# Performance work log

Measured on AMD Instinct MI355X. Metric: run time of the kernel, lower is better.

Reference implementation:

```python
import jax, jax.numpy as jnp
import numpy as np

D_MODEL = 768
N_HEADS = 12
D_HEAD = 64
INIT_RANGE = 0.02
IGNORE = -100000.0


def setup_inputs() -> dict:
    key = jax.random.key(0)
    ks = jax.random.split(key, 5)
    x = jax.random.normal(ks[0], (2, 2048, D_MODEL), dtype=jnp.float32)
    W_Q = INIT_RANGE * jax.random.normal(ks[1], (N_HEADS, D_MODEL, D_HEAD), dtype=jnp.float32)
    W_K = INIT_RANGE * jax.random.normal(ks[2], (N_HEADS, D_MODEL, D_HEAD), dtype=jnp.float32)
    W_V = INIT_RANGE * jax.random.normal(ks[3], (N_HEADS, D_MODEL, D_HEAD), dtype=jnp.float32)
    W_O = INIT_RANGE * jax.random.normal(ks[4], (N_HEADS, D_HEAD, D_MODEL), dtype=jnp.float32)
    b_Q = jnp.zeros((N_HEADS, D_HEAD), dtype=jnp.float32)
    b_K = jnp.zeros((N_HEADS, D_HEAD), dtype=jnp.float32)
    b_V = jnp.zeros((N_HEADS, D_HEAD), dtype=jnp.float32)
    b_O = jnp.zeros((D_MODEL,), dtype=jnp.float32)
    return {"x": x, "W_Q": W_Q, "b_Q": b_Q, "W_K": W_K, "b_K": b_K,
            "W_V": W_V, "b_V": b_V, "W_O": W_O, "b_O": b_O}


def reference(x, W_Q, b_Q, W_K, b_K, W_V, b_V, W_O, b_O):
    # x: [b, s, m]; W_*: [h, m, d]
    Q = jnp.einsum('bsm,hmd->bshd', x, W_Q) + b_Q  # [b, s, h, d]
    K = jnp.einsum('bsm,hmd->bshd', x, W_K) + b_K
    V = jnp.einsum('bsm,hmd->bshd', x, W_V) + b_V
    scores = jnp.einsum('bqhd,bkhd->bhqk', Q, K) / jnp.sqrt(jnp.float32(D_HEAD))
    s = scores.shape[-1]
    causal = jnp.triu(jnp.ones((s, s), dtype=bool), k=1)  # True above diagonal
    scores = jnp.where(causal, jnp.float32(IGNORE), scores)
    pattern = jax.nn.softmax(scores, axis=-1)  # [b, h, q, k]
    Z = jnp.einsum('bhqk,bkhd->bqhd', pattern, V)
    out = jnp.einsum('bqhd,hdm->bqm', Z, W_O) + b_O
    return out
```

## Files before the change

### kernel.cpp

```cpp
#include <hip/hip_runtime.h>
#include <hip/hip_bf16.h>

#define BATCH 2
#define SLEN 2048
#define NH 12
#define DM 768
#define DH 64
#define ROWS (BATCH*SLEN)
#define NQKV (3*DM)
#define NCHUNK 80

typedef __attribute__((ext_vector_type(8))) short bf16x8;
typedef __attribute__((ext_vector_type(4))) float f32x4;
typedef unsigned short u16;
typedef unsigned int u32;
typedef __attribute__((ext_vector_type(4))) unsigned short u16x4;
typedef __attribute__((ext_vector_type(8))) unsigned short u16x8;

__device__ __forceinline__ u16 f2b(float f) {
    unsigned int u = __builtin_bit_cast(unsigned int, f);
    unsigned int r = (u + 0x7FFFu + ((u >> 16) & 1u)) >> 16;
    return (u16)r;
}
__device__ __forceinline__ float b2f(u16 v) {
    unsigned int u = ((unsigned int)v) << 16;
    return __builtin_bit_cast(float, u);
}


__global__ __launch_bounds__(256) void pack_x(const float* __restrict__ x, u16* __restrict__ xb) {
    int i = blockIdx.x * 256 + threadIdx.x;
    const float4* xv = (const float4*)x;
    float4 a = xv[i * 2], b = xv[i * 2 + 1];
    u16x8 o;
    o[0] = f2b(a.x); o[1] = f2b(a.y); o[2] = f2b(a.z); o[3] = f2b(a.w);
    o[4] = f2b(b.x); o[5] = f2b(b.y); o[6] = f2b(b.z); o[7] = f2b(b.w);
    *(u16x8*)(xb + (size_t)i * 8) = o;
}

__global__ __launch_bounds__(256) void pack_wqkv(const float* __restrict__ WQ, const float* __restrict__ WK,
                                                 const float* __restrict__ WV, u16* __restrict__ out) {
    __shared__ u16 L[64 * 72];
    int mt = blockIdx.x, h = blockIdx.y, sel = blockIdx.z;
    const float* W = sel == 0 ? WQ : (sel == 1 ? WK : WV);
    const float* src = W + ((size_t)h * DM + mt * 64) * DH;
    int t = threadIdx.x;
    for (int j = 0; j < 4; j++) {
        int i = t + 256 * j;
        int r = i >> 4, cf = i & 15;
        float4 v = ((const float4*)src)[i];
        u16x4 o; o[0] = f2b(v.x); o[1] = f2b(v.y); o[2] = f2b(v.z); o[3] = f2b(v.w);
        *(u16x4*)&L[r * 72 + cf * 4] = o;
    }
    __syncthreads();
    u16* orow = out + ((size_t)(sel * DM + h * DH)) * DM + mt * 64;
    for (int j = 0; j < 16; j++) {
        int e = t + 256 * j;
        int d = e >> 6, mm = e & 63;
        orow[(size_t)d * DM + mm] = L[mm * 72 + d];
    }
}

__global__ __launch_bounds__(256) void pack_wo(const float* __restrict__ WO, u16* __restrict__ out) {
    __shared__ u16 L[64 * 72];
    int bi = blockIdx.x, bj = blockIdx.y;
    int t = threadIdx.x;
    for (int j = 0; j < 4; j++) {
        int i = t + 256 * j;
        int r = i >> 4, cf = i & 15;
        float4 v = ((const float4*)(WO + (size_t)(bi * 64 + r) * DM + bj * 64))[cf];
        u16x4 o; o[0] = f2b(v.x); o[1] = f2b(v.y); o[2] = f2b(v.z); o[3] = f2b(v.w);
        *(u16x4*)&L[r * 72 + cf * 4] = o;
    }
    __syncthreads();
    for (int j = 0; j < 16; j++) {
        int e = t + 256 * j;
        int c = e >> 6, r = e & 63;
        out[(size_t)(bj * 64 + c) * DM + bi * 64 + r] = L[r * 72 + c];
    }
}


__global__ __launch_bounds__(256) void gemm_qkv(const u16* __restrict__ A, const u16* __restrict__ Bt,
                                                const float* __restrict__ bQ, const float* __restrict__ bK,
                                                const float* __restrict__ bV,
                                                u16* __restrict__ Qb, u16* __restrict__ Kb, u16* __restrict__ Vb) {
    __shared__ u16 Al[128 * 72];
    __shared__ u16 Bl[128 * 72];
    int t = threadIdx.x;
    int n0 = blockIdx.x * 128, m0 = blockIdx.y * 128;
    int lane = t & 63, w = t >> 6;
    int ln = lane & 15, qd = lane >> 4;
    int wr = (w & 1) * 64, wc = (w >> 1) * 64;
    f32x4 acc[4][4] = {};
    for (int kt = 0; kt < DM / 64; kt++) {
        __syncthreads();
        for (int j = 0; j < 4; j++) {
            int i = t + 256 * j;
            int r = i >> 3, cf = i & 7;
            float4 va = *(const float4*)(A + (size_t)(m0 + r) * DM + kt * 64 + cf * 8);
            *(float4*)&Al[r * 72 + cf * 8] = va;
            float4 vb = *(const float4*)(Bt + (size_t)(n0 + r) * DM + kt * 64 + cf * 8);
            *(float4*)&Bl[r * 72 + cf * 8] = vb;
        }
        __syncthreads();
        for (int ks = 0; ks < 2; ks++) {
            bf16x8 af[4], bfr[4];
            for (int rt = 0; rt < 4; rt++)
                af[rt] = *(const bf16x8*)&Al[(wr + rt * 16 + ln) * 72 + ks * 32 + qd * 8];
            for (int ct = 0; ct < 4; ct++)
                bfr[ct] = *(const bf16x8*)&Bl[(wc + ct * 16 + ln) * 72 + ks * 32 + qd * 8];
            for (int rt = 0; rt < 4; rt++)
                for (int ct = 0; ct < 4; ct++)
                    acc[rt][ct] = __builtin_amdgcn_mfma_f32_16x16x32_bf16(af[rt], bfr[ct], acc[rt][ct], 0, 0, 0);
        }
    }
    int sel = n0 / DM;
    if (sel == 2) {
        for (int ct = 0; ct < 4; ct++) {
            int col = n0 - 2 * DM + wc + ct * 16 + ln;
            int hh = col >> 6, dd = col & 63;
            float bv = bV[col];
            for (int rt = 0; rt < 4; rt++) {
                int row = m0 + wr + rt * 16 + qd * 4;
                int bb = row >> 11, ss = row & 2047;
                u16x4 pk;
                for (int r = 0; r < 4; r++) pk[r] = f2b(acc[rt][ct][r] + bv);
                *(u16x4*)&Vb[(((size_t)bb * NH + hh) * DH + dd) * SLEN + ss] = pk;
            }
        }
    } else {
        const float* bias = sel == 0 ? bQ : bK;
        u16* Out = sel == 0 ? Qb : Kb;
        const float qs = sel == 0 ? 0.125f * 1.44269504f : 1.0f;
        for (int ct = 0; ct < 4; ct++) {
            int col = n0 - sel * DM + wc + ct * 16 + ln;
            int hh = col >> 6, dd = col & 63;
            float bv = bias[col];
            for (int rt = 0; rt < 4; rt++) {
                int row = m0 + wr + rt * 16 + qd * 4;
                for (int r = 0; r < 4; r++) {
                    int rg = row + r;
                    int bb = rg >> 11, ss = rg & 2047;
                    Out[(((size_t)bb * NH + hh) * SLEN + ss) * DH + dd] = f2b((acc[rt][ct][r] + bv) * qs);
                }
            }
        }
    }
}


__device__ __forceinline__ void cid2qc(int cid, int& qt, int& c, int& nc) {
    if (cid < 8)       { qt = cid;                 c = 0;              nc = 1; }
    else if (cid < 24) { qt = 8 + ((cid - 8) >> 1); c = (cid - 8) & 1; nc = 2; }
    else if (cid < 48) { qt = 16 + (cid - 24) / 3;  c = (cid - 24) % 3; nc = 3; }
    else               { qt = 24 + ((cid - 48) >> 2); c = (cid - 48) & 3; nc = 4; }
}

__global__ __launch_bounds__(256, 4) void attn(const u16* __restrict__ Qb, const u16* __restrict__ Kb,
                                               const u16* __restrict__ Vtg,
                                               u16* __restrict__ Po, float* __restrict__ Plv) {
    __shared__ u16 Kl[64 * 72];
    __shared__ u16 Vt[64 * 72];
    __shared__ u16 Pq[4][16 * 72];
    int cid = blockIdx.x, bh = blockIdx.y;
    int qt, c, nc;
    cid2qc(cid, qt, c, nc);
    int ntiles = qt + 1;
    int kt0 = c * ntiles / nc, kt1 = (c + 1) * ntiles / nc;
    const u16* Qp = Qb + (size_t)bh * SLEN * DH;
    const u16* Kp = Kb + (size_t)bh * SLEN * DH;
    const u16* Vp = Vtg + (size_t)bh * SLEN * DH;
    int t = threadIdx.x, lane = t & 63, w = t >> 6;
    int ln = lane & 15, qd = lane >> 4;
    int qw = qt * 64 + w * 16;

    bf16x8 qf[2];
    for (int ks = 0; ks < 2; ks++)
        qf[ks] = *(const bf16x8*)(Qp + (size_t)(qw + ln) * DH + ks * 32 + qd * 8);

    float l = 0.f;
    f32x4 o[4] = {};

    u16x8 kr[2], vr[2];
    int sr = t >> 3, scf = t & 7;
    auto preload = [&](int kt) {
        int k0 = kt * 64;
        for (int j = 0; j < 2; j++) {
            int r = sr + 32 * j;
            kr[j] = *(const u16x8*)(Kp + (size_t)(k0 + r) * DH + scf * 8);
            vr[j] = *(const u16x8*)(Vp + (size_t)r * SLEN + k0 + scf * 8);
        }
    };
    preload(kt0);

    u16* Pw = Pq[w];
    for (int kt = kt0; kt < kt1; kt++) {
        __syncthreads();
        for (int j = 0; j < 2; j++) {
            int r = sr + 32 * j;
            *(u16x8*)&Kl[r * 72 + scf * 8] = kr[j];
            *(u16x8*)&Vt[r * 72 + scf * 8] = vr[j];
        }
        __syncthreads();
        if (kt + 1 < kt1) preload(kt + 1);

        f32x4 sf[4] = {};
        for (int ks = 0; ks < 2; ks++)
            for (int ct = 0; ct < 4; ct++) {
                bf16x8 kf = *(const bf16x8*)&Kl[(ct * 16 + ln) * 72 + ks * 32 + qd * 8];
                sf[ct] = __builtin_amdgcn_mfma_f32_16x16x32_bf16(kf, qf[ks], sf[ct], 0, 0, 0);
            }

        if (kt == qt) {
            int qg = qw + ln;
            for (int ct = 0; ct < 4; ct++)
                for (int r = 0; r < 4; r++) {
                    int kg = kt * 64 + ct * 16 + qd * 4 + r;
                    if (kg > qg) sf[ct][r] = -1e30f;
                }
        }

        float s = 0.f;
        for (int ct = 0; ct < 4; ct++) {
            u32 eb[4];
            for (int r = 0; r < 4; r++) {
                float e = exp2f(sf[ct][r]);
                u32 ub = __builtin_bit_cast(u32, e) & 0xFFFF0000u;
                eb[r] = __builtin_bit_cast(u32, e);
                s += __builtin_bit_cast(float, ub);
            }
            u32 p01 = __builtin_amdgcn_perm(eb[1], eb[0], 0x07060302u);
            u32 p23 = __builtin_amdgcn_perm(eb[3], eb[2], 0x07060302u);
            uint2 pk; pk.x = p01; pk.y = p23;
            *(uint2*)&Pw[ln * 72 + ct * 16 + qd * 4] = pk;
        }
        l += s;

        for (int ks = 0; ks < 2; ks++) {
            bf16x8 pf = *(const bf16x8*)&Pw[ln * 72 + ks * 32 + qd * 8];
            for (int dt = 0; dt < 4; dt++) {
                bf16x8 vf = *(const bf16x8*)&Vt[(dt * 16 + ln) * 72 + ks * 32 + qd * 8];
                o[dt] = __builtin_amdgcn_mfma_f32_16x16x32_bf16(vf, pf, o[dt], 0, 0, 0);
            }
        }
    }

    l += __shfl_xor(l, 16, 64);
    l += __shfl_xor(l, 32, 64);

    size_t pid = (size_t)bh * NCHUNK + cid;
    u16* op = Po + pid * 4096;
    for (int dt = 0; dt < 4; dt++) {
        u16x4 ov;
        ov[0] = f2b(o[dt][0]); ov[1] = f2b(o[dt][1]);
        ov[2] = f2b(o[dt][2]); ov[3] = f2b(o[dt][3]);
        *(u16x4*)&op[(w * 16 + ln) * 64 + dt * 16 + qd * 4] = ov;
    }
    if (qd == 0)
        Plv[pid * 64 + w * 16 + ln] = l;
}


__global__ __launch_bounds__(256) void combine(const u16* __restrict__ Po, const float* __restrict__ Plv,
                                               u16* __restrict__ Zb) {
    int qt = blockIdx.x, bh = blockIdx.y;
    int b = bh / NH, h = bh % NH;
    int nc = (qt >> 3) + 1;
    int base;
    if (qt < 8) base = qt;
    else if (qt < 16) base = 8 + (qt - 8) * 2;
    else if (qt < 24) base = 24 + (qt - 16) * 3;
    else base = 48 + (qt - 24) * 4;
    int t = threadIdx.x;
    int q = t >> 2, dseg = (t & 3) * 16;

    float acc[16] = {};
    float lsum = 0.f;
    for (int cc = 0; cc < nc; cc++) {
        size_t pid = (size_t)bh * NCHUNK + base + cc;
        lsum += Plv[pid * 64 + q];
        const u16* op = Po + pid * 4096 + q * 64 + dseg;
        for (int j = 0; j < 2; j++) {
            u16x8 v = *(const u16x8*)(op + j * 8);
            for (int e = 0; e < 8; e++)
                acc[j * 8 + e] += b2f(v[e]);
        }
    }
    float inv = 1.0f / lsum;
    u16* Zp = Zb + ((size_t)b * SLEN + qt * 64 + q) * DM + h * DH + dseg;
    u16x8 ov;
    for (int j = 0; j < 2; j++) {
        for (int e = 0; e < 8; e++) ov[e] = f2b(acc[j * 8 + e] * inv);
        *(u16x8*)(Zp + j * 8) = ov;
    }
}


__global__ __launch_bounds__(256) void gemm_proj(const u16* __restrict__ A, const u16* __restrict__ Bt,
                                                 const float* __restrict__ bO, float* __restrict__ out) {
    __shared__ u16 Al[128 * 72];
    __shared__ u16 Bl[128 * 72];
    int t = threadIdx.x;
    int n0 = blockIdx.x * 128, m0 = blockIdx.y * 128;
    int lane = t & 63, w = t >> 6;
    int ln = lane & 15, qd = lane >> 4;
    int wr = (w & 1) * 64, wc = (w >> 1) * 64;
    f32x4 acc[4][4] = {};
    for (int kt = 0; kt < DM / 64; kt++) {
        __syncthreads();
        for (int j = 0; j < 4; j++) {
            int i = t + 256 * j;
            int r = i >> 3, cf = i & 7;
            float4 va = *(const float4*)(A + (size_t)(m0 + r) * DM + kt * 64 + cf * 8);
            *(float4*)&Al[r * 72 + cf * 8] = va;
            float4 vb = *(const float4*)(Bt + (size_t)(n0 + r) * DM + kt * 64 + cf * 8);
            *(float4*)&Bl[r * 72 + cf * 8] = vb;
        }
        __syncthreads();
        for (int ks = 0; ks < 2; ks++) {
            bf16x8 af[4], bfr[4];
            for (int rt = 0; rt < 4; rt++)
                af[rt] = *(const bf16x8*)&Al[(wr + rt * 16 + ln) * 72 + ks * 32 + qd * 8];
            for (int ct = 0; ct < 4; ct++)
                bfr[ct] = *(const bf16x8*)&Bl[(wc + ct * 16 + ln) * 72 + ks * 32 + qd * 8];
            for (int rt = 0; rt < 4; rt++)
                for (int ct = 0; ct < 4; ct++)
                    acc[rt][ct] = __builtin_amdgcn_mfma_f32_16x16x32_bf16(af[rt], bfr[ct], acc[rt][ct], 0, 0, 0);
        }
    }
    for (int ct = 0; ct < 4; ct++) {
        int col = n0 + wc + ct * 16 + ln;
        float bv = bO[col];
        for (int rt = 0; rt < 4; rt++) {
            int row = m0 + wr + rt * 16 + qd * 4;
            for (int r = 0; r < 4; r++)
                out[(size_t)(row + r) * DM + col] = acc[rt][ct][r] + bv;
        }
    }
}


extern "C" void kernel_launch(void* const* d_in, const int* in_sizes, int n_in,
                              void* d_out, int out_size, void* d_ws, size_t ws_size,
                              hipStream_t stream) {
    const float* x  = (const float*)d_in[0];
    const float* WQ = (const float*)d_in[1];
    const float* bQ = (const float*)d_in[2];
    const float* WK = (const float*)d_in[3];
    const float* bK = (const float*)d_in[4];
    const float* WV = (const float*)d_in[5];
    const float* bV = (const float*)d_in[6];
    const float* WO = (const float*)d_in[7];
    const float* bO = (const float*)d_in[8];
    float* out = (float*)d_out;

    u16* xb   = (u16*)d_ws;
    u16* wqkv = xb + (size_t)ROWS * DM;
    u16* wo   = wqkv + (size_t)NQKV * DM;
    u16* Qb   = wo + (size_t)DM * DM;
    size_t hsz = (size_t)BATCH * NH * SLEN * DH;
    u16* Kb   = Qb + hsz;
    u16* Vb   = Kb + hsz;
    u16* Zb   = Vb + hsz;
    u16* Po   = Zb + (size_t)ROWS * DM;
    float* Pl = (float*)(Po + (size_t)BATCH * NH * NCHUNK * 4096);

    pack_x<<<ROWS * DM / 2048, 256, 0, stream>>>(x, xb);
    pack_wqkv<<<dim3(12, 12, 3), 256, 0, stream>>>(WQ, WK, WV, wqkv);
    pack_wo<<<dim3(12, 12), 256, 0, stream>>>(WO, wo);
    gemm_qkv<<<dim3(NQKV / 128, ROWS / 128), 256, 0, stream>>>(xb, wqkv, bQ, bK, bV, Qb, Kb, Vb);
    attn<<<dim3(NCHUNK, BATCH * NH), 256, 0, stream>>>(Qb, Kb, Vb, Po, Pl);
    combine<<<dim3(SLEN / 64, BATCH * NH), 256, 0, stream>>>(Po, Pl, Zb);
    gemm_proj<<<dim3(DM / 128, ROWS / 128), 256, 0, stream>>>(Zb, wo, bO, out);
}
```

Before: 179.5 us.

## Shrink GEMM N-tiles for more blocks and prefetch next K-tile into registers

The QKV GEMM N-tile goes from 128 to 96 and the output-projection N-tile from 128 to 64. This raises the block count so more of the GPU's compute units stay busy on these small GEMMs. Both GEMMs now load the next K-slice from global memory into registers while MFMAs run on the current shared-memory tile, hiding global load latency. The cost is lower arithmetic intensity per block, more redundant reads of A, and extra registers for the prefetch buffers.

```diff
diff --git a/kernel.cpp b/kernel.cpp
--- a/kernel.cpp
+++ b/kernel.cpp
@@ -86,38 +86,48 @@
                                                 const float* __restrict__ bV,
                                                 u16* __restrict__ Qb, u16* __restrict__ Kb, u16* __restrict__ Vb) {
     __shared__ u16 Al[128 * 72];
-    __shared__ u16 Bl[128 * 72];
-    int t = threadIdx.x;
-    int n0 = blockIdx.x * 128, m0 = blockIdx.y * 128;
+    __shared__ u16 Bl[96 * 72];
+    int t = threadIdx.x;
+    int n0 = blockIdx.x * 96, m0 = blockIdx.y * 128;
     int lane = t & 63, w = t >> 6;
     int ln = lane & 15, qd = lane >> 4;
-    int wr = (w & 1) * 64, wc = (w >> 1) * 64;
-    f32x4 acc[4][4] = {};
+    int wr = (w & 1) * 64, wc = (w >> 1) * 48;
+    int sr = t >> 3, scf = t & 7;
+    f32x4 acc[4][3] = {};
+
+    float4 ar[4], br[3];
+    auto preload = [&](int kt) {
+        const u16* Ap = A + (size_t)m0 * DM + kt * 64;
+        const u16* Bp = Bt + (size_t)n0 * DM + kt * 64;
+        for (int j = 0; j < 4; j++)
+            ar[j] = *(const float4*)(Ap + (size_t)(sr + 32 * j) * DM + scf * 8);
+        for (int j = 0; j < 3; j++)
+            br[j] = *(const float4*)(Bp + (size_t)(sr + 32 * j) * DM + scf * 8);
+    };
+    preload(0);
+
     for (int kt = 0; kt < DM / 64; kt++) {
         __syncthreads();
-        for (int j = 0; j < 4; j++) {
-            int i = t + 256 * j;
-            int r = i >> 3, cf = i & 7;
-            float4 va = *(const float4*)(A + (size_t)(m0 + r) * DM + kt * 64 + cf * 8);
-            *(float4*)&Al[r * 72 + cf * 8] = va;
-            float4 vb = *(const float4*)(Bt + (size_t)(n0 + r) * DM + kt * 64 + cf * 8);
-            *(float4*)&Bl[r * 72 + cf * 8] = vb;
-        }
-        __syncthreads();
+        for (int j = 0; j < 4; j++)
+            *(float4*)&Al[(sr + 32 * j) * 72 + scf * 8] = ar[j];
+        for (int j = 0; j < 3; j++)
+            *(float4*)&Bl[(sr + 32 * j) * 72 + scf * 8] = br[j];
+        __syncthreads();
+        if (kt + 1 < DM / 64) preload(kt + 1);
         for (int ks = 0; ks < 2; ks++) {
-            bf16x8 af[4], bfr[4];
+            bf16x8 af[4], bfr[3];
             for (int rt = 0; rt < 4; rt++)
                 af[rt] = *(const bf16x8*)&Al[(wr + rt * 16 + ln) * 72 + ks * 32 + qd * 8];
-            for (int ct = 0; ct < 4; ct++)
+            for (int ct = 0; ct < 3; ct++)
                 bfr[ct] = *(const bf16x8*)&Bl[(wc + ct * 16 + ln) * 72 + ks * 32 + qd * 8];
             for (int rt = 0; rt < 4; rt++)
-                for (int ct = 0; ct < 4; ct++)
+                for (int ct = 0; ct < 3; ct++)
                     acc[rt][ct] = __builtin_amdgcn_mfma_f32_16x16x32_bf16(af[rt], bfr[ct], acc[rt][ct], 0, 0, 0);
         }
     }
     int sel = n0 / DM;
     if (sel == 2) {
-        for (int ct = 0; ct < 4; ct++) {
+        for (int ct = 0; ct < 3; ct++) {
             int col = n0 - 2 * DM + wc + ct * 16 + ln;
             int hh = col >> 6, dd = col & 63;
             float bv = bV[col];
@@ -133,7 +143,7 @@
         const float* bias = sel == 0 ? bQ : bK;
         u16* Out = sel == 0 ? Qb : Kb;
         const float qs = sel == 0 ? 0.125f * 1.44269504f : 1.0f;
-        for (int ct = 0; ct < 4; ct++) {
+        for (int ct = 0; ct < 3; ct++) {
             int col = n0 - sel * DM + wc + ct * 16 + ln;
             int hh = col >> 6, dd = col & 63;
             float bv = bias[col];
@@ -300,36 +310,46 @@
 __global__ __launch_bounds__(256) void gemm_proj(const u16* __restrict__ A, const u16* __restrict__ Bt,
                                                  const float* __restrict__ bO, float* __restrict__ out) {
     __shared__ u16 Al[128 * 72];
-    __shared__ u16 Bl[128 * 72];
-    int t = threadIdx.x;
-    int n0 = blockIdx.x * 128, m0 = blockIdx.y * 128;
+    __shared__ u16 Bl[64 * 72];
+    int t = threadIdx.x;
+    int n0 = blockIdx.x * 64, m0 = blockIdx.y * 128;
     int lane = t & 63, w = t >> 6;
     int ln = lane & 15, qd = lane >> 4;
-    int wr = (w & 1) * 64, wc = (w >> 1) * 64;
-    f32x4 acc[4][4] = {};
+    int wr = (w & 1) * 64, wc = (w >> 1) * 32;
+    int sr = t >> 3, scf = t & 7;
+    f32x4 acc[4][2] = {};
+
+    float4 ar[4], br[2];
+    auto preload = [&](int kt) {
+        const u16* Ap = A + (size_t)m0 * DM + kt * 64;
+        const u16* Bp = Bt + (size_t)n0 * DM + kt * 64;
+        for (int j = 0; j < 4; j++)
+            ar[j] = *(const float4*)(Ap + (size_t)(sr + 32 * j) * DM + scf * 8);
+        for (int j = 0; j < 2; j++)
+            br[j] = *(const float4*)(Bp + (size_t)(sr + 32 * j) * DM + scf * 8);
+    };
+    preload(0);
+
     for (int kt = 0; kt < DM / 64; kt++) {
         __syncthreads();
-        for (int j = 0; j < 4; j++) {
-            int i = t + 256 * j;
-            int r = i >> 3, cf = i & 7;
-            float4 va = *(const float4*)(A + (size_t)(m0 + r) * DM + kt * 64 + cf * 8);
-            *(float4*)&Al[r * 72 + cf * 8] = va;
-            float4 vb = *(const float4*)(Bt + (size_t)(n0 + r) * DM + kt * 64 + cf * 8);
-            *(float4*)&Bl[r * 72 + cf * 8] = vb;
-        }
-        __syncthreads();
+        for (int j = 0; j < 4; j++)
+            *(float4*)&Al[(sr + 32 * j) * 72 + scf * 8] = ar[j];
+        for (int j = 0; j < 2; j++)
+            *(float4*)&Bl[(sr + 32 * j) * 72 + scf * 8] = br[j];
+        __syncthreads();
+        if (kt + 1 < DM / 64) preload(kt + 1);
         for (int ks = 0; ks < 2; ks++) {
-            bf16x8 af[4], bfr[4];
+            bf16x8 af[4], bfr[2];
             for (int rt = 0; rt < 4; rt++)
                 af[rt] = *(const bf16x8*)&Al[(wr + rt * 16 + ln) * 72 + ks * 32 + qd * 8];
-            for (int ct = 0; ct < 4; ct++)
+            for (int ct = 0; ct < 2; ct++)
                 bfr[ct] = *(const bf16x8*)&Bl[(wc + ct * 16 + ln) * 72 + ks * 32 + qd * 8];
             for (int rt = 0; rt < 4; rt++)
-                for (int ct = 0; ct < 4; ct++)
+                for (int ct = 0; ct < 2; ct++)
                     acc[rt][ct] = __builtin_amdgcn_mfma_f32_16x16x32_bf16(af[rt], bfr[ct], acc[rt][ct], 0, 0, 0);
         }
     }
-    for (int ct = 0; ct < 4; ct++) {
+    for (int ct = 0; ct < 2; ct++) {
         int col = n0 + wc + ct * 16 + ln;
         float bv = bO[col];
         for (int rt = 0; rt < 4; rt++) {
@@ -369,8 +389,8 @@
     pack_x<<<ROWS * DM / 2048, 256, 0, stream>>>(x, xb);
     pack_wqkv<<<dim3(12, 12, 3), 256, 0, stream>>>(WQ, WK, WV, wqkv);
     pack_wo<<<dim3(12, 12), 256, 0, stream>>>(WO, wo);
-    gemm_qkv<<<dim3(NQKV / 128, ROWS / 128), 256, 0, stream>>>(xb, wqkv, bQ, bK, bV, Qb, Kb, Vb);
+    gemm_qkv<<<dim3(NQKV / 96, ROWS / 128), 256, 0, stream>>>(xb, wqkv, bQ, bK, bV, Qb, Kb, Vb);
     attn<<<dim3(NCHUNK, BATCH * NH), 256, 0, stream>>>(Qb, Kb, Vb, Po, Pl);
     combine<<<dim3(SLEN / 64, BATCH * NH), 256, 0, stream>>>(Po, Pl, Zb);
-    gemm_proj<<<dim3(DM / 128, ROWS / 128), 256, 0, stream>>>(Zb, wo, bO, out);
-}
+    gemm_proj<<<dim3(DM / 64, ROWS / 128), 256, 0, stream>>>(Zb, wo, bO, out);
+}
```

After: 250.4 us. 39.5% more time.

## Use direct global-to-LDS loads with XOR swizzle in GEMMs; retile projection

Applied to the files above, without the earlier changes.

Both GEMM kernels now stage A and B tiles with global_load_lds 16-byte direct-to-LDS loads instead of loading into registers and storing to LDS. The padded 72-element row stride is replaced by a 64-wide row with an XOR swizzle of the 16-byte column slots, so MFMA fragment reads avoid bank conflicts. The output projection GEMM is retiled from 128x128 to 64x96 blocks, raising its grid from 192 to 512 workgroups to fill more CUs. Smaller tiles lower per-block reuse and add more global traffic, and the direct LDS path depends on the per-wave contiguous 1 KB destination layout being correct.

```diff
diff --git a/kernel.cpp b/kernel.cpp
--- a/kernel.cpp
+++ b/kernel.cpp
@@ -27,6 +27,13 @@
     return __builtin_bit_cast(float, u);
 }
 
+__device__ __forceinline__ void gload16(const u16* g, u16* l) {
+    __builtin_amdgcn_global_load_lds(
+        (const __attribute__((address_space(1))) unsigned int*)g,
+        (__attribute__((address_space(3))) unsigned int*)l,
+        16, 0, 0);
+}
+
 
 __global__ __launch_bounds__(256) void pack_x(const float* __restrict__ x, u16* __restrict__ xb) {
     int i = blockIdx.x * 256 + threadIdx.x;
@@ -85,31 +92,32 @@
                                                 const float* __restrict__ bQ, const float* __restrict__ bK,
                                                 const float* __restrict__ bV,
                                                 u16* __restrict__ Qb, u16* __restrict__ Kb, u16* __restrict__ Vb) {
-    __shared__ u16 Al[128 * 72];
-    __shared__ u16 Bl[128 * 72];
+    __shared__ u16 Al[128 * 64];
+    __shared__ u16 Bl[128 * 64];
     int t = threadIdx.x;
     int n0 = blockIdx.x * 128, m0 = blockIdx.y * 128;
     int lane = t & 63, w = t >> 6;
     int ln = lane & 15, qd = lane >> 4;
     int wr = (w & 1) * 64, wc = (w >> 1) * 64;
+    int srow = lane >> 3, slot = lane & 7;
     f32x4 acc[4][4] = {};
+
     for (int kt = 0; kt < DM / 64; kt++) {
         __syncthreads();
         for (int j = 0; j < 4; j++) {
-            int i = t + 256 * j;
-            int r = i >> 3, cf = i & 7;
-            float4 va = *(const float4*)(A + (size_t)(m0 + r) * DM + kt * 64 + cf * 8);
-            *(float4*)&Al[r * 72 + cf * 8] = va;
-            float4 vb = *(const float4*)(Bt + (size_t)(n0 + r) * DM + kt * 64 + cf * 8);
-            *(float4*)&Bl[r * 72 + cf * 8] = vb;
+            int r = w * 32 + j * 8 + srow;
+            int gc = slot ^ (r & 7);
+            gload16(A + (size_t)(m0 + r) * DM + kt * 64 + gc * 8, &Al[(w * 32 + j * 8) * 64]);
+            gload16(Bt + (size_t)(n0 + r) * DM + kt * 64 + gc * 8, &Bl[(w * 32 + j * 8) * 64]);
         }
         __syncthreads();
         for (int ks = 0; ks < 2; ks++) {
+            int sl = ((ks * 4 + qd) ^ (ln & 7)) * 8;
             bf16x8 af[4], bfr[4];
             for (int rt = 0; rt < 4; rt++)
-                af[rt] = *(const bf16x8*)&Al[(wr + rt * 16 + ln) * 72 + ks * 32 + qd * 8];
+                af[rt] = *(const bf16x8*)&Al[(wr + rt * 16 + ln) * 64 + sl];
             for (int ct = 0; ct < 4; ct++)
-                bfr[ct] = *(const bf16x8*)&Bl[(wc + ct * 16 + ln) * 72 + ks * 32 + qd * 8];
+                bfr[ct] = *(const bf16x8*)&Bl[(wc + ct * 16 + ln) * 64 + sl];
             for (int rt = 0; rt < 4; rt++)
                 for (int ct = 0; ct < 4; ct++)
                     acc[rt][ct] = __builtin_amdgcn_mfma_f32_16x16x32_bf16(af[rt], bfr[ct], acc[rt][ct], 0, 0, 0);
@@ -299,40 +307,45 @@
 
 __global__ __launch_bounds__(256) void gemm_proj(const u16* __restrict__ A, const u16* __restrict__ Bt,
                                                  const float* __restrict__ bO, float* __restrict__ out) {
-    __shared__ u16 Al[128 * 72];
-    __shared__ u16 Bl[128 * 72];
-    int t = threadIdx.x;
-    int n0 = blockIdx.x * 128, m0 = blockIdx.y * 128;
+    __shared__ u16 Al[64 * 64];
+    __shared__ u16 Bl[96 * 64];
+    int t = threadIdx.x;
+    int n0 = blockIdx.x * 96, m0 = blockIdx.y * 64;
     int lane = t & 63, w = t >> 6;
     int ln = lane & 15, qd = lane >> 4;
-    int wr = (w & 1) * 64, wc = (w >> 1) * 64;
-    f32x4 acc[4][4] = {};
+    int wr = (w & 1) * 32, wc = (w >> 1) * 48;
+    int srow = lane >> 3, slot = lane & 7;
+    f32x4 acc[2][3] = {};
+
     for (int kt = 0; kt < DM / 64; kt++) {
         __syncthreads();
-        for (int j = 0; j < 4; j++) {
-            int i = t + 256 * j;
-            int r = i >> 3, cf = i & 7;
-            float4 va = *(const float4*)(A + (size_t)(m0 + r) * DM + kt * 64 + cf * 8);
-            *(float4*)&Al[r * 72 + cf * 8] = va;
-            float4 vb = *(const float4*)(Bt + (size_t)(n0 + r) * DM + kt * 64 + cf * 8);
-            *(float4*)&Bl[r * 72 + cf * 8] = vb;
+        for (int j = 0; j < 2; j++) {
+            int r = w * 16 + j * 8 + srow;
+            int gc = slot ^ (r & 7);
+            gload16(A + (size_t)(m0 + r) * DM + kt * 64 + gc * 8, &Al[(w * 16 + j * 8) * 64]);
+        }
+        for (int j = 0; j < 3; j++) {
+            int r = w * 24 + j * 8 + srow;
+            int gc = slot ^ (r & 7);
+            gload16(Bt + (size_t)(n0 + r) * DM + kt * 64 + gc * 8, &Bl[(w * 24 + j * 8) * 64]);
         }
         __syncthreads();
         for (int ks = 0; ks < 2; ks++) {
-            bf16x8 af[4], bfr[4];
-            for (int rt = 0; rt < 4; rt++)
-                af[rt] = *(const bf16x8*)&Al[(wr + rt * 16 + ln) * 72 + ks * 32 + qd * 8];
-            for (int ct = 0; ct < 4; ct++)
-                bfr[ct] = *(const bf16x8*)&Bl[(wc + ct * 16 + ln) * 72 + ks * 32 + qd * 8];
-            for (int rt = 0; rt < 4; rt++)
-                for (int ct = 0; ct < 4; ct++)
+            int sl = ((ks * 4 + qd) ^ (ln & 7)) * 8;
+            bf16x8 af[2], bfr[3];
+            for (int rt = 0; rt < 2; rt++)
+                af[rt] = *(const bf16x8*)&Al[(wr + rt * 16 + ln) * 64 + sl];
+            for (int ct = 0; ct < 3; ct++)
+                bfr[ct] = *(const bf16x8*)&Bl[(wc + ct * 16 + ln) * 64 + sl];
+            for (int rt = 0; rt < 2; rt++)
+                for (int ct = 0; ct < 3; ct++)
                     acc[rt][ct] = __builtin_amdgcn_mfma_f32_16x16x32_bf16(af[rt], bfr[ct], acc[rt][ct], 0, 0, 0);
         }
     }
-    for (int ct = 0; ct < 4; ct++) {
+    for (int ct = 0; ct < 3; ct++) {
         int col = n0 + wc + ct * 16 + ln;
         float bv = bO[col];
-        for (int rt = 0; rt < 4; rt++) {
+        for (int rt = 0; rt < 2; rt++) {
             int row = m0 + wr + rt * 16 + qd * 4;
             for (int r = 0; r < 4; r++)
                 out[(size_t)(row + r) * DM + col] = acc[rt][ct][r] + bv;
@@ -372,5 +385,5 @@
     gemm_qkv<<<dim3(NQKV / 128, ROWS / 128), 256, 0, stream>>>(xb, wqkv, bQ, bK, bV, Qb, Kb, Vb);
     attn<<<dim3(NCHUNK, BATCH * NH), 256, 0, stream>>>(Qb, Kb, Vb, Po, Pl);
     combine<<<dim3(SLEN / 64, BATCH * NH), 256, 0, stream>>>(Po, Pl, Zb);
-    gemm_proj<<<dim3(DM / 128, ROWS / 128), 256, 0, stream>>>(Zb, wo, bO, out);
-}
+    gemm_proj<<<dim3(DM / 96, ROWS / 64), 256, 0, stream>>>(Zb, wo, bO, out);
+}
```

After: 173.5 us. 3.4% less time.
